# Kernel tuning notes

Measured on AMD Instinct MI355X. Metric: run time of the kernel, lower is better.

The kernel has to match this reference:

```python
import jax, jax.numpy as jnp
import numpy as np

DECAY = 0.99
EPS = 1e-05


def setup_inputs() -> dict:
    key = jax.random.key(0)
    k1, k2, k3, k4 = jax.random.split(key, 4)
    B, T, D, K = 16, 4096, 128, 1024
    return {
        "z": jax.random.normal(k1, (B, T, D), dtype=jnp.float32),
        "embedding": jax.random.normal(k2, (K, D), dtype=jnp.float32),
        "cluster_size": jax.random.uniform(k3, (K,), dtype=jnp.float32),
        "ema_w": jax.random.normal(k4, (K, D), dtype=jnp.float32),
    }


def reference(z, embedding, cluster_size, ema_w):
    B, T, D = z.shape
    K = embedding.shape[0]
    z_flat = z.reshape(B * T, D)

    # Squared-distance matrix [N, K]: ||z||^2 - 2 z E^T + ||E||^2
    dist = (
        jnp.sum(z_flat * z_flat, axis=1, keepdims=True)
        - 2.0 * (z_flat @ embedding.T)
        + jnp.sum(embedding * embedding, axis=1)
    )
    indices = jnp.argmin(dist, axis=1)  # [N]
    z_q = embedding[indices].reshape(B, T, D)

    # EMA codebook update (training branch); segment_sum == one_hot.T @ z, one_hot.sum(0)
    batch_cluster = jax.ops.segment_sum(
        jnp.ones((B * T,), dtype=z.dtype), indices, num_segments=K
    )
    new_cluster_size = cluster_size * DECAY + (1.0 - DECAY) * batch_cluster
    batch_ema = jax.ops.segment_sum(z_flat, indices, num_segments=K)
    new_ema_w = ema_w * DECAY + (1.0 - DECAY) * batch_ema

    n = jnp.sum(new_cluster_size)
    smoothed = (new_cluster_size + EPS) / (n + K * EPS) * n
    new_embedding = new_ema_w / smoothed[:, None]

    # Commitment loss on OLD codebook vectors (matches torch order of ops)
    loss_vq = jnp.mean(jnp.square(jax.lax.stop_gradient(z_q) - z))
    # Straight-through estimator
    z_q_st = z + jax.lax.stop_gradient(z_q - z)

    return (
        z_q_st,
        indices.reshape(B, T),
        loss_vq,
        new_embedding,
        new_cluster_size,
        new_ema_w,
    )
```

## Files before the change

kernel.cpp:

```cpp
#include <hip/hip_runtime.h>

#define K_CODES 1024
#define D_DIM 128
#define N_ROWS 65536
#define DECAY_F 0.99f
#define OMD_F 0.01f
#define EPS_F 1e-5f

#define EPAD 144
#define CHUNK_CODES 64
#define N_CHUNKS 16
#define CHUNK_USHORT (2 * CHUNK_CODES * EPAD)
#define NT 2
#define SEG_TILE 128

#define WS_CNT     0
#define WS_LOSS    1024
#define WS_BE      1028
#define WS_ZERO_END (1028 + 131072)
#define WS_ENORM   132100
#define WS_SMOOTH  133124
#define WS_CUR     134148
#define WS_FIDX    135172
#define WS_BUCKET  200708
#define WS_EIMG    331780

typedef __bf16 bf8_t __attribute__((ext_vector_type(8)));
typedef float  f4_t  __attribute__((ext_vector_type(4)));

__device__ inline unsigned short f2bf_bits(float f) {
    __bf16 h = (__bf16)f;
    return __builtin_bit_cast(unsigned short, h);
}
__device__ inline float bf_bits2f(unsigned short u) {
    __bf16 h = __builtin_bit_cast(__bf16, u);
    return (float)h;
}

__device__ inline void gld16(const void* g, void* l) {
    __builtin_amdgcn_global_load_lds(
        (const __attribute__((address_space(1))) void*)g,
        (__attribute__((address_space(3))) void*)l, 16, 0, 0);
}

__global__ void vq_prep(const float* __restrict__ emb, float* __restrict__ enorm,
                        unsigned short* __restrict__ eimg,
                        float4* __restrict__ zero_head, float4* __restrict__ zero_be) {
    int t = blockIdx.x * blockDim.x + threadIdx.x;
    float4 z4 = {0.f, 0.f, 0.f, 0.f};
    if (t < 257) zero_head[t] = z4;
    zero_be[t] = z4;

    int code = t >> 5;
    int q = t & 31;
    float4 v = ((const float4*)(emb + (size_t)code * D_DIM))[q];
    int chunk = code >> 6, c = code & 63;
    size_t hbase = (size_t)chunk * CHUNK_USHORT + (size_t)c * EPAD + q * 4;
    size_t lbase = hbase + (size_t)CHUNK_CODES * EPAD;
    float vv[4] = {v.x, v.y, v.z, v.w};
    ushort4 hi, lo;
    unsigned short* hp = (unsigned short*)&hi;
    unsigned short* lp = (unsigned short*)&lo;
#pragma unroll
    for (int i = 0; i < 4; ++i) {
        unsigned short hb = f2bf_bits(vv[i]);
        hp[i] = hb;
        lp[i] = f2bf_bits(vv[i] - bf_bits2f(hb));
    }
    *(ushort4*)(eimg + hbase) = hi;
    *(ushort4*)(eimg + lbase) = lo;

    float s = v.x * v.x + v.y * v.y + v.z * v.z + v.w * v.w;
#pragma unroll
    for (int o = 1; o < 32; o <<= 1) s += __shfl_xor(s, o, 64);
    if (q == 0) enorm[code] = s;
}

__device__ inline void top2_update(float s, int code, float& s1, int& i1, float& s2, int& i2) {
    bool b1 = s < s1;
    bool b2 = s < s2;
    s2 = b1 ? s1 : (b2 ? s : s2);
    i2 = b1 ? i1 : (b2 ? code : i2);
    s1 = b1 ? s : s1;
    i1 = b1 ? code : i1;
}

__device__ inline void top2_merge(float& s1, int& i1, float& s2, int& i2,
                                  float t1, int j1, float t2, int j2) {
    bool bf = (t1 < s1) || (t1 == s1 && j1 < i1);
    float ns1 = bf ? t1 : s1;  int ni1 = bf ? j1 : i1;
    float ca  = bf ? s1 : t1;  int ia  = bf ? i1 : j1;
    float cb  = bf ? t2 : s2;  int ib  = bf ? j2 : i2;
    bool bs = (ca < cb) || (ca == cb && ia < ib);
    s1 = ns1; i1 = ni1;
    s2 = bs ? ca : cb; i2 = bs ? ia : ib;
}

__global__ __launch_bounds__(256) void vq_score(
    const float* __restrict__ z, const unsigned short* __restrict__ eimg,
    const float* __restrict__ enorm_g, const float* __restrict__ emb,
    float* __restrict__ out_zq, float* __restrict__ out_idx,
    int* __restrict__ cnt, unsigned int* __restrict__ fidx,
    float* __restrict__ loss_acc)
{
    __shared__ __align__(16) unsigned short lds[2][CHUNK_USHORT];
    __shared__ __align__(16) float lds_en[K_CODES];

    const int tid  = threadIdx.x;
    const int wv   = tid >> 6;
    const int lane = tid & 63;
    const int l16  = lane & 15;
    const int quad = lane >> 4;
    const int rowbase = blockIdx.x * 128 + wv * 32;

    ((float4*)lds_en)[tid] = ((const float4*)enorm_g)[tid];

    {
        const char* gs = (const char*)eimg;
        char* ls = (char*)&lds[0][0];
        int wb = wv * 9216;
#pragma unroll
        for (int i = 0; i < 9; ++i)
            gld16(gs + wb + i * 1024 + lane * 16, ls + wb + i * 1024);
    }

    bf8_t zh[NT][4], zl[NT][4];
#pragma unroll
    for (int nt = 0; nt < NT; ++nt) {
        int row = rowbase + nt * 16 + l16;
        const float* zr = z + (size_t)row * D_DIM;
#pragma unroll
        for (int ks = 0; ks < 4; ++ks) {
            const float4* p = (const float4*)(zr + ks * 32 + quad * 8);
            float4 a = p[0], b = p[1];
            float v[8] = {a.x, a.y, a.z, a.w, b.x, b.y, b.z, b.w};
#pragma unroll
            for (int i = 0; i < 8; ++i) {
                __bf16 hh = (__bf16)v[i];
                zh[nt][ks][i] = hh;
                zl[nt][ks][i] = (__bf16)(v[i] - (float)hh);
            }
        }
    }

    float s1[NT], s2[NT];
    int   i1[NT], i2[NT];
#pragma unroll
    for (int nt = 0; nt < NT; ++nt) { s1[nt] = 3.4e38f; s2[nt] = 3.4e38f; i1[nt] = 0; i2[nt] = 0; }

    __syncthreads();

    for (int c = 0; c < N_CHUNKS; ++c) {
        const int cur = c & 1;
        if (c + 1 < N_CHUNKS) {
            const char* gs = (const char*)(eimg + (size_t)(c + 1) * CHUNK_USHORT);
            char* ls = (char*)&lds[1 - cur][0];
            int wb = wv * 9216;
#pragma unroll
            for (int i = 0; i < 9; ++i)
                gld16(gs + wb + i * 1024 + lane * 16, ls + wb + i * 1024);
        }
        const unsigned short* buf = &lds[cur][0];

#pragma unroll
        for (int cg = 0; cg < 2; ++cg) {
            f4_t acc[2][NT];
#pragma unroll
            for (int ct = 0; ct < 2; ++ct)
#pragma unroll
                for (int nt = 0; nt < NT; ++nt) acc[ct][nt] = (f4_t)(0.f);

#pragma unroll
            for (int ks = 0; ks < 4; ++ks) {
                bf8_t ah[2], al[2];
#pragma unroll
                for (int ct = 0; ct < 2; ++ct) {
                    int cl = cg * 32 + ct * 16 + l16;
                    int base = cl * EPAD + ks * 32 + quad * 8;
                    ah[ct] = *(const bf8_t*)&buf[base];
                    al[ct] = *(const bf8_t*)&buf[CHUNK_CODES * EPAD + base];
                }
#pragma unroll
                for (int ct = 0; ct < 2; ++ct)
#pragma unroll
                    for (int nt = 0; nt < NT; ++nt) {
                        acc[ct][nt] = __builtin_amdgcn_mfma_f32_16x16x32_bf16(
                            ah[ct], zh[nt][ks], acc[ct][nt], 0, 0, 0);
                        acc[ct][nt] = __builtin_amdgcn_mfma_f32_16x16x32_bf16(
                            al[ct], zh[nt][ks], acc[ct][nt], 0, 0, 0);
                        acc[ct][nt] = __builtin_amdgcn_mfma_f32_16x16x32_bf16(
                            ah[ct], zl[nt][ks], acc[ct][nt], 0, 0, 0);
                    }
            }

#pragma unroll
            for (int ct = 0; ct < 2; ++ct) {
                int cb = c * 64 + cg * 32 + ct * 16 + quad * 4;
                float4 en4 = *(const float4*)&lds_en[cb];
                float env[4] = {en4.x, en4.y, en4.z, en4.w};
#pragma unroll
                for (int nt = 0; nt < NT; ++nt)
#pragma unroll
                    for (int r = 0; r < 4; ++r) {
                        float s = env[r] - 2.0f * acc[ct][nt][r];
                        top2_update(s, cb + r, s1[nt], i1[nt], s2[nt], i2[nt]);
                    }
            }
        }
        __syncthreads();
    }

#pragma unroll
    for (int off = 16; off <= 32; off <<= 1) {
#pragma unroll
        for (int nt = 0; nt < NT; ++nt) {
            float t1 = __shfl_xor(s1[nt], off, 64);
            int   j1 = __shfl_xor(i1[nt], off, 64);
            float t2 = __shfl_xor(s2[nt], off, 64);
            int   j2 = __shfl_xor(i2[nt], off, 64);
            top2_merge(s1[nt], i1[nt], s2[nt], i2[nt], t1, j1, t2, j2);
        }
    }

    float ls = 0.f;
#pragma unroll
    for (int nt = 0; nt < NT; ++nt) {
        int row = rowbase + nt * 16 + l16;
        int j1 = i1[nt], j2 = i2[nt];

        const float4* zp  = (const float4*)(z   + (size_t)row * D_DIM);
        const float4* e1p = (const float4*)(emb + (size_t)j1  * D_DIM);
        const float4* e2p = (const float4*)(emb + (size_t)j2  * D_DIM);

        float4 zv[8], a1[8], a2[8];
#pragma unroll
        for (int ks = 0; ks < 4; ++ks) {
            int o = ks * 8 + quad * 2;
            zv[ks * 2]     = zp[o];   zv[ks * 2 + 1] = zp[o + 1];
            a1[ks * 2]     = e1p[o];  a1[ks * 2 + 1] = e1p[o + 1];
            a2[ks * 2]     = e2p[o];  a2[ks * 2 + 1] = e2p[o + 1];
        }
        float p1 = 0.f, p2 = 0.f;
#pragma unroll
        for (int i = 0; i < 8; ++i) {
            p1 += zv[i].x * a1[i].x + zv[i].y * a1[i].y + zv[i].z * a1[i].z + zv[i].w * a1[i].w;
            p2 += zv[i].x * a2[i].x + zv[i].y * a2[i].y + zv[i].z * a2[i].z + zv[i].w * a2[i].w;
        }
        p1 += __shfl_xor(p1, 16, 64); p1 += __shfl_xor(p1, 32, 64);
        p2 += __shfl_xor(p2, 16, 64); p2 += __shfl_xor(p2, 32, 64);
        float sc1 = lds_en[j1] - 2.0f * p1;
        float sc2 = lds_en[j2] - 2.0f * p2;
        bool use2 = (sc2 < sc1) || (sc2 == sc1 && j2 < j1);
        int best = use2 ? j2 : j1;

        if (quad == 0) {
            out_idx[row] = (float)best;
            fidx[row] = (unsigned int)best;
            atomicAdd(cnt + best, 1);
        }

        float4* oz = (float4*)(out_zq + (size_t)row * D_DIM);
#pragma unroll
        for (int i = 0; i < 8; ++i) {
            float4 q = use2 ? a2[i] : a1[i];
            float4 zvv = zv[i];
            float4 df = {q.x - zvv.x, q.y - zvv.y, q.z - zvv.z, q.w - zvv.w};
            ls += df.x * df.x + df.y * df.y + df.z * df.z + df.w * df.w;
            float4 o = {zvv.x + df.x, zvv.y + df.y, zvv.z + df.z, zvv.w + df.w};
            oz[(i >> 1) * 8 + quad * 2 + (i & 1)] = o;
        }
    }

#pragma unroll
    for (int off = 32; off > 0; off >>= 1) ls += __shfl_down(ls, off, 64);
    if (lane == 0) atomicAdd(loss_acc, ls);
}

__global__ void vq_scan(const int* __restrict__ cnt, int* __restrict__ cursor,
                        const float* __restrict__ cs, const float* __restrict__ lacc,
                        float* __restrict__ out_ncs, float* __restrict__ out_loss,
                        float* __restrict__ smoothed)
{
    __shared__ int   wsum[16];
    __shared__ float fr[16];
    int k = threadIdx.x;
    int wv = k >> 6, lane = k & 63;
    int c = cnt[k];

    int x = c;
#pragma unroll
    for (int off = 1; off < 64; off <<= 1) {
        int t = __shfl_up(x, off, 64);
        if (lane >= off) x += t;
    }
    if (lane == 63) wsum[wv] = x;

    float ncs = cs[k] * DECAY_F + OMD_F * (float)c;
    out_ncs[k] = ncs;
    float s = ncs;
#pragma unroll
    for (int o = 1; o < 64; o <<= 1) s += __shfl_xor(s, o, 64);
    if (lane == 0) fr[wv] = s;
    __syncthreads();

    int woff = 0; float n = 0.f;
#pragma unroll
    for (int i = 0; i < 16; ++i) {
        if (i < wv) woff += wsum[i];
        n += fr[i];
    }
    cursor[k] = woff + x - c;
    smoothed[k] = (ncs + EPS_F) / (n + (float)K_CODES * EPS_F) * n;
    if (k == 0) out_loss[0] = lacc[0] / (float)((size_t)N_ROWS * D_DIM);
}

__global__ void vq_scatter(const unsigned int* __restrict__ fidx,
                           int* __restrict__ cursor,
                           unsigned long long* __restrict__ packed)
{
    int row = blockIdx.x * blockDim.x + threadIdx.x;
    int k = (int)fidx[row];
    int slot = atomicAdd(cursor + k, 1);
    packed[slot] = ((unsigned long long)(unsigned)k << 32) | (unsigned)row;
}

__global__ __launch_bounds__(128) void vq_segsum(
    const float* __restrict__ z, const unsigned long long* __restrict__ packed,
    float* __restrict__ be)
{
    __shared__ int sb[SEG_TILE];
    __shared__ int sc[SEG_TILE];
    const int tid = threadIdx.x;
    const int t0  = blockIdx.x * SEG_TILE;

    {
        unsigned long long v = packed[t0 + tid];
        sb[tid] = (int)(unsigned)(v & 0xffffffffu);
        sc[tid] = (int)(v >> 32);
    }
    __syncthreads();

    const int d = tid;
    float acc = 0.f;
    int cur = sc[0];

    for (int i = 0; i < SEG_TILE; i += 8) {
        float v[8];
#pragma unroll
        for (int j = 0; j < 8; ++j)
            v[j] = z[(size_t)sb[i + j] * D_DIM + d];
#pragma unroll
        for (int j = 0; j < 8; ++j) {
            int c = sc[i + j];
            if (c != cur) {
                atomicAdd(be + (size_t)cur * D_DIM + d, acc);
                acc = 0.f;
                cur = c;
            }
            acc += v[j];
        }
    }
    atomicAdd(be + (size_t)cur * D_DIM + d, acc);
}

__global__ void vq_finalize2(const float* __restrict__ ema_w, const float* __restrict__ be,
                             const float* __restrict__ smoothed,
                             float* __restrict__ out_emb, float* __restrict__ out_ema)
{
    int i = blockIdx.x * blockDim.x + threadIdx.x;
    float e = ema_w[i] * DECAY_F + OMD_F * be[i];
    out_ema[i] = e;
    out_emb[i] = e / smoothed[i >> 7];
}

extern "C" void kernel_launch(void* const* d_in, const int* in_sizes, int n_in,
                              void* d_out, int out_size, void* d_ws, size_t ws_size,
                              hipStream_t stream) {
    const float* z   = (const float*)d_in[0];
    const float* emb = (const float*)d_in[1];
    const float* cs  = (const float*)d_in[2];
    const float* ema = (const float*)d_in[3];

    float* out    = (float*)d_out;
    float* o_zq   = out;
    float* o_idx  = o_zq + (size_t)N_ROWS * D_DIM;
    float* o_loss = o_idx + N_ROWS;
    float* o_emb  = o_loss + 1;
    float* o_ncs  = o_emb + K_CODES * D_DIM;
    float* o_ema  = o_ncs + K_CODES;

    float* ws = (float*)d_ws;
    int*                 cnt      = (int*)(ws + WS_CNT);
    float*               lacc     = ws + WS_LOSS;
    float*               be       = ws + WS_BE;
    float*               enorm    = ws + WS_ENORM;
    float*               smoothed = ws + WS_SMOOTH;
    int*                 cursor   = (int*)(ws + WS_CUR);
    unsigned int*        fidx     = (unsigned int*)(ws + WS_FIDX);
    unsigned long long*  packed   = (unsigned long long*)(ws + WS_BUCKET);
    unsigned short*      eimg     = (unsigned short*)(ws + WS_EIMG);

    vq_prep<<<128, 256, 0, stream>>>(emb, enorm, eimg,
                                     (float4*)(ws + WS_CNT), (float4*)(ws + WS_BE));
    vq_score<<<512, 256, 0, stream>>>(z, eimg, enorm, emb,
                                      o_zq, o_idx, cnt, fidx, lacc);
    vq_scan<<<1, K_CODES, 0, stream>>>(cnt, cursor, cs, lacc, o_ncs, o_loss, smoothed);
    vq_scatter<<<N_ROWS / 256, 256, 0, stream>>>(fidx, cursor, packed);
    vq_segsum<<<N_ROWS / SEG_TILE, 128, 0, stream>>>(z, packed, be);
    vq_finalize2<<<K_CODES * D_DIM / 256, 256, 0, stream>>>(ema, be, smoothed, o_emb, o_ema);
}
```

Measured before the change: 214.2 us.

## Read codebook directly from global memory instead of LDS double-buffering

Removes the LDS staging of the bf16 hi/lo codebook image and the norm table, so each single-wave block reads codebook fragments straight from global memory (through L1/L2). It also unpads the codebook layout and relaunches the kernel with 64-thread blocks, four times as many blocks. The aim is to cut the LDS traffic and block-wide barriers and let occupancy hide latency. The cost is that every wave now fetches the whole 512KB codebook image through the cache hierarchy with no sharing across waves in LDS.

```diff
diff --git a/kernel.cpp b/kernel.cpp
--- a/kernel.cpp
+++ b/kernel.cpp
@@ -7,17 +7,14 @@
 #define OMD_F 0.01f
 #define EPS_F 1e-5f
 
-#define EPAD 144
-#define CHUNK_CODES 64
 #define N_CHUNKS 16
-#define CHUNK_USHORT (2 * CHUNK_CODES * EPAD)
 #define NT 2
 #define SEG_TILE 128
+#define EIMG_LO 131072
 
 #define WS_CNT     0
 #define WS_LOSS    1024
 #define WS_BE      1028
-#define WS_ZERO_END (1028 + 131072)
 #define WS_ENORM   132100
 #define WS_SMOOTH  133124
 #define WS_CUR     134148
@@ -35,12 +32,6 @@
 __device__ inline float bf_bits2f(unsigned short u) {
     __bf16 h = __builtin_bit_cast(__bf16, u);
     return (float)h;
-}
-
-__device__ inline void gld16(const void* g, void* l) {
-    __builtin_amdgcn_global_load_lds(
-        (const __attribute__((address_space(1))) void*)g,
-        (__attribute__((address_space(3))) void*)l, 16, 0, 0);
 }
 
 __global__ void vq_prep(const float* __restrict__ emb, float* __restrict__ enorm,
@@ -54,9 +45,7 @@
     int code = t >> 5;
     int q = t & 31;
     float4 v = ((const float4*)(emb + (size_t)code * D_DIM))[q];
-    int chunk = code >> 6, c = code & 63;
-    size_t hbase = (size_t)chunk * CHUNK_USHORT + (size_t)c * EPAD + q * 4;
-    size_t lbase = hbase + (size_t)CHUNK_CODES * EPAD;
+    size_t hbase = (size_t)code * 128 + q * 4;
     float vv[4] = {v.x, v.y, v.z, v.w};
     ushort4 hi, lo;
     unsigned short* hp = (unsigned short*)&hi;
@@ -68,7 +57,7 @@
         lp[i] = f2bf_bits(vv[i] - bf_bits2f(hb));
     }
     *(ushort4*)(eimg + hbase) = hi;
-    *(ushort4*)(eimg + lbase) = lo;
+    *(ushort4*)(eimg + EIMG_LO + hbase) = lo;
 
     float s = v.x * v.x + v.y * v.y + v.z * v.z + v.w * v.w;
 #pragma unroll
@@ -96,33 +85,18 @@
     s2 = bs ? ca : cb; i2 = bs ? ia : ib;
 }
 
-__global__ __launch_bounds__(256) void vq_score(
+__global__ __launch_bounds__(64, 3) void vq_score(
     const float* __restrict__ z, const unsigned short* __restrict__ eimg,
     const float* __restrict__ enorm_g, const float* __restrict__ emb,
     float* __restrict__ out_zq, float* __restrict__ out_idx,
     int* __restrict__ cnt, unsigned int* __restrict__ fidx,
     float* __restrict__ loss_acc)
 {
-    __shared__ __align__(16) unsigned short lds[2][CHUNK_USHORT];
-    __shared__ __align__(16) float lds_en[K_CODES];
-
-    const int tid  = threadIdx.x;
-    const int wv   = tid >> 6;
-    const int lane = tid & 63;
+    const int lane = threadIdx.x & 63;
     const int l16  = lane & 15;
     const int quad = lane >> 4;
-    const int rowbase = blockIdx.x * 128 + wv * 32;
-
-    ((float4*)lds_en)[tid] = ((const float4*)enorm_g)[tid];
-
-    {
-        const char* gs = (const char*)eimg;
-        char* ls = (char*)&lds[0][0];
-        int wb = wv * 9216;
-#pragma unroll
-        for (int i = 0; i < 9; ++i)
-            gld16(gs + wb + i * 1024 + lane * 16, ls + wb + i * 1024);
-    }
+    const int rowbase = blockIdx.x * 32;
+    const int off0 = l16 * 128 + quad * 8;
 
     bf8_t zh[NT][4], zl[NT][4];
 #pragma unroll
@@ -148,20 +122,7 @@
 #pragma unroll
     for (int nt = 0; nt < NT; ++nt) { s1[nt] = 3.4e38f; s2[nt] = 3.4e38f; i1[nt] = 0; i2[nt] = 0; }
 
-    __syncthreads();
-
     for (int c = 0; c < N_CHUNKS; ++c) {
-        const int cur = c & 1;
-        if (c + 1 < N_CHUNKS) {
-            const char* gs = (const char*)(eimg + (size_t)(c + 1) * CHUNK_USHORT);
-            char* ls = (char*)&lds[1 - cur][0];
-            int wb = wv * 9216;
-#pragma unroll
-            for (int i = 0; i < 9; ++i)
-                gld16(gs + wb + i * 1024 + lane * 16, ls + wb + i * 1024);
-        }
-        const unsigned short* buf = &lds[cur][0];
-
 #pragma unroll
         for (int cg = 0; cg < 2; ++cg) {
             f4_t acc[2][NT];
@@ -175,10 +136,9 @@
                 bf8_t ah[2], al[2];
 #pragma unroll
                 for (int ct = 0; ct < 2; ++ct) {
-                    int cl = cg * 32 + ct * 16 + l16;
-                    int base = cl * EPAD + ks * 32 + quad * 8;
-                    ah[ct] = *(const bf8_t*)&buf[base];
-                    al[ct] = *(const bf8_t*)&buf[CHUNK_CODES * EPAD + base];
+                    int cbase = (c * 64 + cg * 32 + ct * 16) * 128;
+                    ah[ct] = *(const bf8_t*)&eimg[cbase + off0 + ks * 32];
+                    al[ct] = *(const bf8_t*)&eimg[EIMG_LO + cbase + off0 + ks * 32];
                 }
 #pragma unroll
                 for (int ct = 0; ct < 2; ++ct)
@@ -196,7 +156,7 @@
 #pragma unroll
             for (int ct = 0; ct < 2; ++ct) {
                 int cb = c * 64 + cg * 32 + ct * 16 + quad * 4;
-                float4 en4 = *(const float4*)&lds_en[cb];
+                float4 en4 = *(const float4*)&enorm_g[cb];
                 float env[4] = {en4.x, en4.y, en4.z, en4.w};
 #pragma unroll
                 for (int nt = 0; nt < NT; ++nt)
@@ -207,7 +167,6 @@
                     }
             }
         }
-        __syncthreads();
     }
 
 #pragma unroll
@@ -248,8 +207,8 @@
         }
         p1 += __shfl_xor(p1, 16, 64); p1 += __shfl_xor(p1, 32, 64);
         p2 += __shfl_xor(p2, 16, 64); p2 += __shfl_xor(p2, 32, 64);
-        float sc1 = lds_en[j1] - 2.0f * p1;
-        float sc2 = lds_en[j2] - 2.0f * p2;
+        float sc1 = enorm_g[j1] - 2.0f * p1;
+        float sc2 = enorm_g[j2] - 2.0f * p2;
         bool use2 = (sc2 < sc1) || (sc2 == sc1 && j2 < j1);
         int best = use2 ? j2 : j1;
 
@@ -402,7 +361,7 @@
 
     vq_prep<<<128, 256, 0, stream>>>(emb, enorm, eimg,
                                      (float4*)(ws + WS_CNT), (float4*)(ws + WS_BE));
-    vq_score<<<512, 256, 0, stream>>>(z, eimg, enorm, emb,
+    vq_score<<<2048, 64, 0, stream>>>(z, eimg, enorm, emb,
                                       o_zq, o_idx, cnt, fidx, lacc);
     vq_scan<<<1, K_CODES, 0, stream>>>(cnt, cursor, cs, lacc, o_ncs, o_loss, smoothed);
     vq_scatter<<<N_ROWS / 256, 256, 0, stream>>>(fidx, cursor, packed);
```

Result: slower. 297.5 us (+38.9%).

## Halve per-wave row tile and codebook chunk to raise vq_score occupancy

Applied to the files above, without the earlier changes.

Each wave now scores 16 rows instead of 32, and the codebook is streamed in 32-code chunks instead of 64, so LDS use and register pressure per block drop and launch bounds request 4 blocks per CU. The grid doubles to 1024 blocks. The aim is more resident waves to hide LDS and global latency. In exchange, each codebook tile loaded into LDS is reused by half as many rows, so global and LDS traffic per row doubles, and there are twice as many chunk barriers.

```diff
diff --git a/kernel.cpp b/kernel.cpp
--- a/kernel.cpp
+++ b/kernel.cpp
@@ -8,16 +8,15 @@
 #define EPS_F 1e-5f
 
 #define EPAD 144
-#define CHUNK_CODES 64
-#define N_CHUNKS 16
+#define CHUNK_CODES 32
+#define N_CHUNKS 32
 #define CHUNK_USHORT (2 * CHUNK_CODES * EPAD)
-#define NT 2
+#define CHUNK_BYTES 18432
 #define SEG_TILE 128
 
 #define WS_CNT     0
 #define WS_LOSS    1024
 #define WS_BE      1028
-#define WS_ZERO_END (1028 + 131072)
 #define WS_ENORM   132100
 #define WS_SMOOTH  133124
 #define WS_CUR     134148
@@ -54,7 +53,7 @@
     int code = t >> 5;
     int q = t & 31;
     float4 v = ((const float4*)(emb + (size_t)code * D_DIM))[q];
-    int chunk = code >> 6, c = code & 63;
+    int chunk = code >> 5, c = code & 31;
     size_t hbase = (size_t)chunk * CHUNK_USHORT + (size_t)c * EPAD + q * 4;
     size_t lbase = hbase + (size_t)CHUNK_CODES * EPAD;
     float vv[4] = {v.x, v.y, v.z, v.w};
@@ -96,7 +95,7 @@
     s2 = bs ? ca : cb; i2 = bs ? ia : ib;
 }
 
-__global__ __launch_bounds__(256) void vq_score(
+__global__ __launch_bounds__(256, 4) void vq_score(
     const float* __restrict__ z, const unsigned short* __restrict__ eimg,
     const float* __restrict__ enorm_g, const float* __restrict__ emb,
     float* __restrict__ out_zq, float* __restrict__ out_idx,
@@ -111,23 +110,22 @@
     const int lane = tid & 63;
     const int l16  = lane & 15;
     const int quad = lane >> 4;
-    const int rowbase = blockIdx.x * 128 + wv * 32;
+    const int row  = blockIdx.x * 64 + wv * 16 + l16;
 
     ((float4*)lds_en)[tid] = ((const float4*)enorm_g)[tid];
 
     {
         const char* gs = (const char*)eimg;
         char* ls = (char*)&lds[0][0];
-        int wb = wv * 9216;
-#pragma unroll
-        for (int i = 0; i < 9; ++i)
-            gld16(gs + wb + i * 1024 + lane * 16, ls + wb + i * 1024);
-    }
-
-    bf8_t zh[NT][4], zl[NT][4];
-#pragma unroll
-    for (int nt = 0; nt < NT; ++nt) {
-        int row = rowbase + nt * 16 + l16;
+#pragma unroll
+        for (int i = 0; i < 5; ++i) {
+            int idx = wv + 4 * i;
+            if (idx < 18) gld16(gs + idx * 1024 + lane * 16, ls + idx * 1024);
+        }
+    }
+
+    bf8_t zh[4], zl[4];
+    {
         const float* zr = z + (size_t)row * D_DIM;
 #pragma unroll
         for (int ks = 0; ks < 4; ++ks) {
@@ -137,74 +135,60 @@
 #pragma unroll
             for (int i = 0; i < 8; ++i) {
                 __bf16 hh = (__bf16)v[i];
-                zh[nt][ks][i] = hh;
-                zl[nt][ks][i] = (__bf16)(v[i] - (float)hh);
-            }
-        }
-    }
-
-    float s1[NT], s2[NT];
-    int   i1[NT], i2[NT];
-#pragma unroll
-    for (int nt = 0; nt < NT; ++nt) { s1[nt] = 3.4e38f; s2[nt] = 3.4e38f; i1[nt] = 0; i2[nt] = 0; }
+                zh[ks][i] = hh;
+                zl[ks][i] = (__bf16)(v[i] - (float)hh);
+            }
+        }
+    }
+
+    float s1 = 3.4e38f, s2 = 3.4e38f;
+    int   i1 = 0, i2 = 0;
 
     __syncthreads();
 
     for (int c = 0; c < N_CHUNKS; ++c) {
         const int cur = c & 1;
         if (c + 1 < N_CHUNKS) {
-            const char* gs = (const char*)(eimg + (size_t)(c + 1) * CHUNK_USHORT);
+            const char* gs = (const char*)eimg + (size_t)(c + 1) * CHUNK_BYTES;
             char* ls = (char*)&lds[1 - cur][0];
-            int wb = wv * 9216;
-#pragma unroll
-            for (int i = 0; i < 9; ++i)
-                gld16(gs + wb + i * 1024 + lane * 16, ls + wb + i * 1024);
+#pragma unroll
+            for (int i = 0; i < 5; ++i) {
+                int idx = wv + 4 * i;
+                if (idx < 18) gld16(gs + idx * 1024 + lane * 16, ls + idx * 1024);
+            }
         }
         const unsigned short* buf = &lds[cur][0];
 
-#pragma unroll
-        for (int cg = 0; cg < 2; ++cg) {
-            f4_t acc[2][NT];
-#pragma unroll
-            for (int ct = 0; ct < 2; ++ct)
-#pragma unroll
-                for (int nt = 0; nt < NT; ++nt) acc[ct][nt] = (f4_t)(0.f);
-
-#pragma unroll
-            for (int ks = 0; ks < 4; ++ks) {
-                bf8_t ah[2], al[2];
-#pragma unroll
-                for (int ct = 0; ct < 2; ++ct) {
-                    int cl = cg * 32 + ct * 16 + l16;
-                    int base = cl * EPAD + ks * 32 + quad * 8;
-                    ah[ct] = *(const bf8_t*)&buf[base];
-                    al[ct] = *(const bf8_t*)&buf[CHUNK_CODES * EPAD + base];
-                }
-#pragma unroll
-                for (int ct = 0; ct < 2; ++ct)
-#pragma unroll
-                    for (int nt = 0; nt < NT; ++nt) {
-                        acc[ct][nt] = __builtin_amdgcn_mfma_f32_16x16x32_bf16(
-                            ah[ct], zh[nt][ks], acc[ct][nt], 0, 0, 0);
-                        acc[ct][nt] = __builtin_amdgcn_mfma_f32_16x16x32_bf16(
-                            al[ct], zh[nt][ks], acc[ct][nt], 0, 0, 0);
-                        acc[ct][nt] = __builtin_amdgcn_mfma_f32_16x16x32_bf16(
-                            ah[ct], zl[nt][ks], acc[ct][nt], 0, 0, 0);
-                    }
-            }
-
+        f4_t acc[2];
+        acc[0] = (f4_t)(0.f); acc[1] = (f4_t)(0.f);
+
+#pragma unroll
+        for (int ks = 0; ks < 4; ++ks) {
+            bf8_t ah[2], al[2];
 #pragma unroll
             for (int ct = 0; ct < 2; ++ct) {
-                int cb = c * 64 + cg * 32 + ct * 16 + quad * 4;
-                float4 en4 = *(const float4*)&lds_en[cb];
-                float env[4] = {en4.x, en4.y, en4.z, en4.w};
-#pragma unroll
-                for (int nt = 0; nt < NT; ++nt)
-#pragma unroll
-                    for (int r = 0; r < 4; ++r) {
-                        float s = env[r] - 2.0f * acc[ct][nt][r];
-                        top2_update(s, cb + r, s1[nt], i1[nt], s2[nt], i2[nt]);
-                    }
+                int cl = ct * 16 + l16;
+                int base = cl * EPAD + ks * 32 + quad * 8;
+                ah[ct] = *(const bf8_t*)&buf[base];
+                al[ct] = *(const bf8_t*)&buf[CHUNK_CODES * EPAD + base];
+            }
+#pragma unroll
+            for (int ct = 0; ct < 2; ++ct) {
+                acc[ct] = __builtin_amdgcn_mfma_f32_16x16x32_bf16(ah[ct], zh[ks], acc[ct], 0, 0, 0);
+                acc[ct] = __builtin_amdgcn_mfma_f32_16x16x32_bf16(al[ct], zh[ks], acc[ct], 0, 0, 0);
+                acc[ct] = __builtin_amdgcn_mfma_f32_16x16x32_bf16(ah[ct], zl[ks], acc[ct], 0, 0, 0);
+            }
+        }
+
+#pragma unroll
+        for (int ct = 0; ct < 2; ++ct) {
+            int cb = c * 32 + ct * 16 + quad * 4;
+            float4 en4 = *(const float4*)&lds_en[cb];
+            float env[4] = {en4.x, en4.y, en4.z, en4.w};
+#pragma unroll
+            for (int r = 0; r < 4; ++r) {
+                float s = env[r] - 2.0f * acc[ct][r];
+                top2_update(s, cb + r, s1, i1, s2, i2);
             }
         }
         __syncthreads();
@@ -212,21 +196,16 @@
 
 #pragma unroll
     for (int off = 16; off <= 32; off <<= 1) {
-#pragma unroll
-        for (int nt = 0; nt < NT; ++nt) {
-            float t1 = __shfl_xor(s1[nt], off, 64);
-            int   j1 = __shfl_xor(i1[nt], off, 64);
-            float t2 = __shfl_xor(s2[nt], off, 64);
-            int   j2 = __shfl_xor(i2[nt], off, 64);
-            top2_merge(s1[nt], i1[nt], s2[nt], i2[nt], t1, j1, t2, j2);
-        }
+        float t1 = __shfl_xor(s1, off, 64);
+        int   j1 = __shfl_xor(i1, off, 64);
+        float t2 = __shfl_xor(s2, off, 64);
+        int   j2 = __shfl_xor(i2, off, 64);
+        top2_merge(s1, i1, s2, i2, t1, j1, t2, j2);
     }
 
     float ls = 0.f;
-#pragma unroll
-    for (int nt = 0; nt < NT; ++nt) {
-        int row = rowbase + nt * 16 + l16;
-        int j1 = i1[nt], j2 = i2[nt];
+    {
+        int j1 = i1, j2 = i2;
 
         const float4* zp  = (const float4*)(z   + (size_t)row * D_DIM);
         const float4* e1p = (const float4*)(emb + (size_t)j1  * D_DIM);
@@ -402,8 +381,8 @@
 
     vq_prep<<<128, 256, 0, stream>>>(emb, enorm, eimg,
                                      (float4*)(ws + WS_CNT), (float4*)(ws + WS_BE));
-    vq_score<<<512, 256, 0, stream>>>(z, eimg, enorm, emb,
-                                      o_zq, o_idx, cnt, fidx, lacc);
+    vq_score<<<1024, 256, 0, stream>>>(z, eimg, enorm, emb,
+                                       o_zq, o_idx, cnt, fidx, lacc);
     vq_scan<<<1, K_CODES, 0, stream>>>(cnt, cursor, cs, lacc, o_ncs, o_loss, smoothed);
     vq_scatter<<<N_ROWS / 256, 256, 0, stream>>>(fidx, cursor, packed);
     vq_segsum<<<N_ROWS / SEG_TILE, 128, 0, stream>>>(z, packed, be);
```

Result: slower. 234.8 us (+9.6%).
